# Optimization experiments

Hardware: AMD Instinct MI355X
Metric: run time of the kernel (lower is better)

The kernel has to match this reference:

```python
import jax, jax.numpy as jnp
import numpy as np

B, S, D, P = 8, 2048, 512, 64  # batch, seq, num_embed_hidden, num_attention_project


def setup_inputs() -> dict:
    key = jax.random.key(0)
    ks = jax.random.split(key, 9)
    sd = 1.0 / np.sqrt(D)
    sp = 1.0 / np.sqrt(P)
    return {
        "query": jax.random.normal(ks[0], (B, S, D), dtype=jnp.float32),
        "attention_mask": jnp.ones((B, S), dtype=jnp.float32),
        "Wq": jax.random.uniform(ks[1], (D, P), jnp.float32, -sd, sd),
        "bq": jax.random.uniform(ks[2], (P,), jnp.float32, -sd, sd),
        "Wk": jax.random.uniform(ks[3], (D, P), jnp.float32, -sd, sd),
        "bk": jax.random.uniform(ks[4], (P,), jnp.float32, -sd, sd),
        "Wv": jax.random.uniform(ks[5], (D, P), jnp.float32, -sd, sd),
        "bv": jax.random.uniform(ks[6], (P,), jnp.float32, -sd, sd),
        "Wo": jax.random.uniform(ks[7], (P, D), jnp.float32, -sp, sp),
        "bo": jax.random.uniform(ks[8], (D,), jnp.float32, -sp, sp),
    }


def reference(query, attention_mask, Wq, bq, Wk, bk, Wv, bv, Wo, bo):
    q = jnp.einsum("bsd,dp->bsp", query, Wq) + bq  # [B,S,P]
    k = jnp.einsum("bsd,dp->bsp", query, Wk) + bk
    v = jnp.einsum("bsd,dp->bsp", query, Wv) + bv
    scores = jnp.einsum("bsp,btp->bst", q, k) / jnp.sqrt(jnp.float32(P))  # [B,S,S]
    # Faithful to original: mask broadcast over last axis via unsqueeze(-1) -> masks rows
    scores = scores + (1.0 - attention_mask[:, :, None]) * -10000.0
    weights = jax.nn.softmax(scores, axis=-1)
    weighted = jnp.einsum("bst,btp->bsp", weights, v)
    return jnp.einsum("bsp,pd->bsd", weighted, Wo) + bo
```

## Files before the change

kernel.cpp:

```cpp
#include <hip/hip_runtime.h>
#include <hip/hip_bf16.h>
#include <math.h>

constexpr int B = 8;
constexpr int S = 2048;
constexpr int D = 512;
constexpr int P = 64;
constexpr float SCALE = 0.125f;

typedef short bf16x8 __attribute__((ext_vector_type(8)));
typedef short s16x4 __attribute__((ext_vector_type(4)));
typedef float f32x4 __attribute__((ext_vector_type(4)));

__device__ __forceinline__ unsigned short f2bf(float x) {
  __hip_bfloat16 h = __float2bfloat16(x);
  return __builtin_bit_cast(unsigned short, h);
}
__device__ __forceinline__ float bf2f(unsigned short u) {
  unsigned int v = (unsigned int)u << 16;
  return __builtin_bit_cast(float, v);
}


__global__ __launch_bounds__(256) void prep_w(
    const float* __restrict__ Wq, const float* __restrict__ Wk,
    const float* __restrict__ Wv, const float* __restrict__ Wo,
    unsigned short* __restrict__ Bfrag, unsigned short* __restrict__ Wofrag) {
  const int i = blockIdx.x * 256 + threadIdx.x;
  if (i < 192 * 512) {
    const int d = i / 192;
    const int n = i - d * 192;
    const float* W = (n < 64) ? Wq : (n < 128) ? Wk : Wv;
    const float val = W[d * 64 + (n & 63)];
    const int nt = n >> 4, l15 = n & 15;
    const int k16 = d >> 5, l4 = (d >> 3) & 3, j = d & 7;
    Bfrag[(((nt * 16 + k16) * 4 + l4) * 16 + l15) * 8 + j] = f2bf(val);
  }
  if (i < 64 * 512) {
    const int k = i >> 9;
    const int n = i & 511;
    const float val = Wo[k * 512 + n];
    const int ct = n >> 4, l15 = n & 15;
    const int h = k >> 5, l4 = (k >> 3) & 3, j = k & 7;
    Wofrag[(((ct * 2 + h) * 4 + l4) * 16 + l15) * 8 + j] = f2bf(val);
  }
}

__global__ __launch_bounds__(256)
__attribute__((amdgpu_waves_per_eu(4, 4))) void qkv_mfma(
    const float* __restrict__ query, const unsigned short* __restrict__ Bfrag,
    const float* __restrict__ bq, const float* __restrict__ bk,
    const float* __restrict__ bv, unsigned short* __restrict__ qfrag,
    unsigned short* __restrict__ kfrag, unsigned short* __restrict__ vfrag) {
  __shared__ __align__(16) unsigned short Aq[16 * 512];

  const int tid = threadIdx.x;
  const int w = tid >> 6;
  const int l = tid & 63;
  const int l15 = l & 15;
  const int l4 = l >> 4;
  const int s0 = blockIdx.x * 16;
  const int kb0 = blockIdx.x & 15;

  const float* qsrc = query + (size_t)s0 * D;
#pragma unroll
  for (int step = 0; step < 4; ++step) {
    const int row = step * 4 + w;
    const float* pf = qsrc + row * D + l * 8;
    const float4 x = *(const float4*)pf;
    const float4 y = *(const float4*)(pf + 4);
    bf16x8 u;
    u[0] = (short)f2bf(x.x); u[1] = (short)f2bf(x.y);
    u[2] = (short)f2bf(x.z); u[3] = (short)f2bf(x.w);
    u[4] = (short)f2bf(y.x); u[5] = (short)f2bf(y.y);
    u[6] = (short)f2bf(y.z); u[7] = (short)f2bf(y.w);
    *(bf16x8*)&Aq[row * 512 + ((l ^ (row & 7)) << 3)] = u;
  }
  __syncthreads();

  f32x4 acc[3];
#pragma unroll
  for (int m = 0; m < 3; ++m) acc[m] = (f32x4){0.f, 0.f, 0.f, 0.f};

#pragma unroll
  for (int kk = 0; kk < 16; ++kk) {
    const int k16 = (kk + kb0) & 15;
    const int aslot = (k16 * 4 + l4) ^ (l15 & 7);
    const bf16x8 af = *(const bf16x8*)&Aq[l15 * 512 + (aslot << 3)];
    const bf16x8 bfq =
        *(const bf16x8*)(Bfrag + ((size_t)(w * 16 + k16) * 64 + l) * 8);
    const bf16x8 bfk =
        *(const bf16x8*)(Bfrag + ((size_t)((4 + w) * 16 + k16) * 64 + l) * 8);
    const bf16x8 bfv =
        *(const bf16x8*)(Bfrag + ((size_t)((8 + w) * 16 + k16) * 64 + l) * 8);
    acc[0] = __builtin_amdgcn_mfma_f32_16x16x32_bf16(bfq, af, acc[0], 0, 0, 0);
    acc[1] = __builtin_amdgcn_mfma_f32_16x16x32_bf16(bfk, af, acc[1], 0, 0, 0);
    acc[2] = __builtin_amdgcn_mfma_f32_16x16x32_bf16(af, bfv, acc[2], 0, 0, 0);
  }

  const int bidx = s0 >> 11;
  const size_t bbase = (size_t)bidx * (S * P);
  const int S0 = s0 & 2047;

  const int p0 = w * 16 + l4 * 4;
  const float4 bq4 = *(const float4*)(bq + p0);
  const float4 bk4 = *(const float4*)(bk + p0);
  const size_t qkoff =
      bbase +
      ((((size_t)(S0 >> 4) * 2 + (p0 >> 5)) * 4 + ((p0 >> 3) & 3)) * 16 +
       l15) * 8 +
      (p0 & 7);
  s16x4 pq, pkk;
  pq[0] = (short)f2bf((acc[0][0] + bq4.x) * SCALE);
  pq[1] = (short)f2bf((acc[0][1] + bq4.y) * SCALE);
  pq[2] = (short)f2bf((acc[0][2] + bq4.z) * SCALE);
  pq[3] = (short)f2bf((acc[0][3] + bq4.w) * SCALE);
  pkk[0] = (short)f2bf(acc[1][0] + bk4.x);
  pkk[1] = (short)f2bf(acc[1][1] + bk4.y);
  pkk[2] = (short)f2bf(acc[1][2] + bk4.z);
  pkk[3] = (short)f2bf(acc[1][3] + bk4.w);
  *(s16x4*)(qfrag + qkoff) = pq;
  *(s16x4*)(kfrag + qkoff) = pkk;

  const float bbv = bv[w * 16 + l15];
  const int chv = ((S0 >> 3) + (l4 >> 1)) & 3;
  const size_t voff =
      bbase + ((((size_t)(S0 >> 5) * 4 + w) * 4 + chv) * 16 + l15) * 8 +
      (l4 & 1) * 4;
  s16x4 pv;
  pv[0] = (short)f2bf(acc[2][0] + bbv);
  pv[1] = (short)f2bf(acc[2][1] + bbv);
  pv[2] = (short)f2bf(acc[2][2] + bbv);
  pv[3] = (short)f2bf(acc[2][3] + bbv);
  *(s16x4*)(vfrag + voff) = pv;
}

__global__ __launch_bounds__(1024)
__attribute__((amdgpu_waves_per_eu(4, 4))) void attn_fused(
    const unsigned short* __restrict__ qfrag,
    const unsigned short* __restrict__ kfrag,
    const unsigned short* __restrict__ vfrag,
    const unsigned short* __restrict__ Wofrag, const float* __restrict__ bo,
    float* __restrict__ out) {
  __shared__ __align__(16) unsigned char smem[131072];
  __shared__ float l_s[16][32];

  const int tid = threadIdx.x;
  const int w = tid >> 6;
  const int lane = tid & 63;
  const int l15 = lane & 15;
  const int l4 = lane >> 4;
  const int qg = w & 1;
  const int th = w >> 1;

  const int blk = blockIdx.x;
  const int b = blk & 7;
  const int qt = blk >> 3;
  const int s0 = qt * 64;
  const int wst = qt & 3;

  const size_t bbase = (size_t)b * (S * P);
  const unsigned short* qf = qfrag + bbase;
  const unsigned short* kf = kfrag + bbase;
  const unsigned short* vf = vfrag + bbase;

  unsigned char* e_w = smem + w * 8192;
  const int xm = (l15 & 7) << 4;

  bf16x8 aq[2][2];
#pragma unroll
  for (int st = 0; st < 2; ++st)
#pragma unroll
    for (int h = 0; h < 2; ++h)
      aq[st][h] =
          *(const bf16x8*)(qf +
                           ((size_t)(((s0 >> 4) + qg * 2 + st) * 2 + h) * 64 +
                            lane) *
                               8);

  f32x4 acc[2][4];
#pragma unroll
  for (int st = 0; st < 2; ++st)
#pragma unroll
    for (int pc = 0; pc < 4; ++pc) acc[st][pc] = (f32x4){0.f, 0.f, 0.f, 0.f};
  float lpart[2] = {0.f, 0.f};

  for (int win = 0; win < 4; ++win) {
    const int wi = (win + wst) & 3;
    const int t0 = th * 256 + wi * 64;
    unsigned char* epb = e_w + (win & 1) * 4096;

#pragma unroll 1
    for (int hf = 0; hf < 2; ++hf) {
      bf16x8 bkh[2][2];
#pragma unroll
      for (int j = 0; j < 2; ++j)
#pragma unroll
        for (int h = 0; h < 2; ++h)
          bkh[j][h] =
              *(const bf16x8*)(kf + ((size_t)(((t0 >> 4) + hf * 2 + j) * 2 +
                                              h) * 64 + lane) * 8);

#pragma unroll
      for (int st = 0; st < 2; ++st) {
        f32x4 sc[2];
#pragma unroll
        for (int j = 0; j < 2; ++j) {
          f32x4 c = (f32x4){0.f, 0.f, 0.f, 0.f};
          c = __builtin_amdgcn_mfma_f32_16x16x32_bf16(bkh[j][0], aq[st][0], c,
                                                      0, 0, 0);
          sc[j] = __builtin_amdgcn_mfma_f32_16x16x32_bf16(bkh[j][1], aq[st][1],
                                                          c, 0, 0, 0);
        }
#pragma unroll
        for (int j = 0; j < 2; ++j) {
          s16x4 pk;
#pragma unroll
          for (int r = 0; r < 4; ++r) pk[r] = (short)f2bf(__expf(sc[j][r]));
#pragma unroll
          for (int r = 0; r < 4; ++r)
            lpart[st] += bf2f((unsigned short)pk[r]);
          *(s16x4*)(epb + st * 2048 + l15 * 128 +
                    (((hf * 2 + j) * 32 + l4 * 8) ^ xm)) = pk;
        }
      }

      bf16x8 bvh[4];
#pragma unroll
      for (int pc = 0; pc < 4; ++pc)
        bvh[pc] =
            *(const bf16x8*)(vf + ((size_t)(((t0 >> 5) + hf) * 4 + pc) * 64 +
                                   lane) * 8);

#pragma unroll
      for (int st = 0; st < 2; ++st) {
        const bf16x8 ae = *(const bf16x8*)(epb + st * 2048 + l15 * 128 +
                                           ((hf * 64 + l4 * 16) ^ xm));
#pragma unroll
        for (int pc = 0; pc < 4; ++pc)
          acc[st][pc] = __builtin_amdgcn_mfma_f32_16x16x32_bf16(
              ae, bvh[pc], acc[st][pc], 0, 0, 0);
      }
    }
  }

#pragma unroll
  for (int st = 0; st < 2; ++st) {
    float v = lpart[st];
    v += __shfl_xor(v, 16, 64);
    v += __shfl_xor(v, 32, 64);
    if (l4 == 0) l_s[w][st * 16 + l15] = v;
  }

  __syncthreads();

  float* pacc = (float*)smem;
#pragma unroll
  for (int st = 0; st < 2; ++st)
#pragma unroll
    for (int pc = 0; pc < 4; ++pc)
#pragma unroll
      for (int r = 0; r < 4; ++r) {
        const int row = st * 16 + l4 * 4 + r;
        pacc[((size_t)w * 32 + row) * 64 + ((pc ^ l4) * 16) + l15] =
            acc[st][pc][r];
      }
  __syncthreads();

  const int R = w * 4 + l4;
  const int qgR = R >> 5;
  const int r32 = R & 31;
  const int csw = (r32 >> 2) & 3;
  const int coff = (((l15 >> 2) ^ csw) * 16) + (l15 & 3) * 4;
  float4 s4 = {0.f, 0.f, 0.f, 0.f};
#pragma unroll
  for (int t8 = 0; t8 < 8; ++t8) {
    const float4 p4 =
        *(const float4*)&pacc[((size_t)(t8 * 2 + qgR) * 32 + r32) * 64 + coff];
    s4.x += p4.x; s4.y += p4.y; s4.z += p4.z; s4.w += p4.w;
  }
  float ls = 0.f;
#pragma unroll
  for (int t8 = 0; t8 < 8; ++t8) ls += l_s[t8 * 2 + qgR][r32];
  const float inv = 1.f / ls;
  s16x4 wn;
  wn[0] = (short)f2bf(s4.x * inv);
  wn[1] = (short)f2bf(s4.y * inv);
  wn[2] = (short)f2bf(s4.z * inv);
  wn[3] = (short)f2bf(s4.w * inv);
  __syncthreads();

  unsigned short* wnorm = (unsigned short*)smem;
  *(s16x4*)&wnorm[R * 64 + l15 * 4] = wn;
  __syncthreads();

  const int sub = w & 3;
  const int chq = w >> 2;
  const bf16x8 a0 = *(const bf16x8*)&wnorm[(sub * 16 + l15) * 64 + l4 * 8];
  const bf16x8 a1 =
      *(const bf16x8*)&wnorm[(sub * 16 + l15) * 64 + 32 + l4 * 8];
  const size_t orow0 = (size_t)b * S + s0 + sub * 16;
#pragma unroll
  for (int ct = 0; ct < 8; ++ct) {
    const int ctg = chq * 8 + ((ct + (blk & 7)) & 7);
    const bf16x8 b0 =
        *(const bf16x8*)(Wofrag + ((size_t)(ctg * 2 + 0) * 64 + lane) * 8);
    const bf16x8 b1 =
        *(const bf16x8*)(Wofrag + ((size_t)(ctg * 2 + 1) * 64 + lane) * 8);
    f32x4 c = (f32x4){0.f, 0.f, 0.f, 0.f};
    c = __builtin_amdgcn_mfma_f32_16x16x32_bf16(a0, b0, c, 0, 0, 0);
    c = __builtin_amdgcn_mfma_f32_16x16x32_bf16(a1, b1, c, 0, 0, 0);
    const int col = ctg * 16 + l15;
    const float bb = bo[col];
#pragma unroll
    for (int r = 0; r < 4; ++r)
      out[(orow0 + l4 * 4 + r) * D + col] = c[r] + bb;
  }
}

extern "C" void kernel_launch(void* const* d_in, const int* in_sizes, int n_in,
                              void* d_out, int out_size, void* d_ws,
                              size_t ws_size, hipStream_t stream) {
  const float* query = (const float*)d_in[0];
  const float* Wq = (const float*)d_in[2];
  const float* bq = (const float*)d_in[3];
  const float* Wk = (const float*)d_in[4];
  const float* bk = (const float*)d_in[5];
  const float* Wv = (const float*)d_in[6];
  const float* bv = (const float*)d_in[7];
  const float* Wo = (const float*)d_in[8];
  const float* bo = (const float*)d_in[9];
  float* out = (float*)d_out;

  const size_t proj = (size_t)B * S * P;
  unsigned short* qfr = (unsigned short*)d_ws;
  unsigned short* kfr = qfr + proj;
  unsigned short* vfr = kfr + proj;
  unsigned short* Bfrag = vfr + proj;
  unsigned short* Wofrag = Bfrag + 192 * 512;

  prep_w<<<384, 256, 0, stream>>>(Wq, Wk, Wv, Wo, Bfrag, Wofrag);
  qkv_mfma<<<1024, 256, 0, stream>>>(query, Bfrag, bq, bk, bv, qfr, kfr, vfr);
  attn_fused<<<256, 1024, 0, stream>>>(qfr, kfr, vfr, Wofrag, bo, out);
}
```

Baseline: 124.1 us.

## Halve query tile per block to double grid and cut LDS use

The attention kernel now processes 32 query rows per block instead of 64. Each of the 16 waves covers a distinct 128-key slice, and 512 blocks are launched instead of 256. The cross-wave reduction of partial outputs now runs in two phases over column halves, so LDS drops from 128KB to about 68KB and the waves-per-EU hint is relaxed. The aim is to let two blocks share a CU and to fill all CUs on a 256-CU part. In exchange, each block loads K/V twice as often per query row, adds a barrier-separated reduction phase, and loses the double-buffered exp staging.

```diff
diff --git a/kernel.cpp b/kernel.cpp
--- a/kernel.cpp
+++ b/kernel.cpp
@@ -136,13 +136,13 @@
 }
 
 __global__ __launch_bounds__(1024)
-__attribute__((amdgpu_waves_per_eu(4, 4))) void attn_fused(
+__attribute__((amdgpu_waves_per_eu(8))) void attn_fused(
     const unsigned short* __restrict__ qfrag,
     const unsigned short* __restrict__ kfrag,
     const unsigned short* __restrict__ vfrag,
     const unsigned short* __restrict__ Wofrag, const float* __restrict__ bo,
     float* __restrict__ out) {
-  __shared__ __align__(16) unsigned char smem[131072];
+  __shared__ __align__(16) unsigned char smem[69632];
   __shared__ float l_s[16][32];
 
   const int tid = threadIdx.x;
@@ -150,21 +150,19 @@
   const int lane = tid & 63;
   const int l15 = lane & 15;
   const int l4 = lane >> 4;
-  const int qg = w & 1;
-  const int th = w >> 1;
 
   const int blk = blockIdx.x;
   const int b = blk & 7;
   const int qt = blk >> 3;
-  const int s0 = qt * 64;
-  const int wst = qt & 3;
+  const int s0 = qt * 32;
+  const int wst = qt & 1;
 
   const size_t bbase = (size_t)b * (S * P);
   const unsigned short* qf = qfrag + bbase;
   const unsigned short* kf = kfrag + bbase;
   const unsigned short* vf = vfrag + bbase;
 
-  unsigned char* e_w = smem + w * 8192;
+  unsigned char* e_w = smem + w * 4096;
   const int xm = (l15 & 7) << 4;
 
   bf16x8 aq[2][2];
@@ -174,9 +172,7 @@
     for (int h = 0; h < 2; ++h)
       aq[st][h] =
           *(const bf16x8*)(qf +
-                           ((size_t)(((s0 >> 4) + qg * 2 + st) * 2 + h) * 64 +
-                            lane) *
-                               8);
+                           ((size_t)((qt * 2 + st) * 2 + h) * 64 + lane) * 8);
 
   f32x4 acc[2][4];
 #pragma unroll
@@ -185,10 +181,10 @@
     for (int pc = 0; pc < 4; ++pc) acc[st][pc] = (f32x4){0.f, 0.f, 0.f, 0.f};
   float lpart[2] = {0.f, 0.f};
 
-  for (int win = 0; win < 4; ++win) {
-    const int wi = (win + wst) & 3;
-    const int t0 = th * 256 + wi * 64;
-    unsigned char* epb = e_w + (win & 1) * 4096;
+  for (int win = 0; win < 2; ++win) {
+    const int wi = (win + wst) & 1;
+    const int t0 = w * 128 + wi * 64;
+    unsigned char* epb = e_w;
 
 #pragma unroll 1
     for (int hf = 0; hf < 2; ++hf) {
@@ -255,54 +251,48 @@
   __syncthreads();
 
   float* pacc = (float*)smem;
-#pragma unroll
-  for (int st = 0; st < 2; ++st)
-#pragma unroll
-    for (int pc = 0; pc < 4; ++pc)
-#pragma unroll
-      for (int r = 0; r < 4; ++r) {
-        const int row = st * 16 + l4 * 4 + r;
-        pacc[((size_t)w * 32 + row) * 64 + ((pc ^ l4) * 16) + l15] =
-            acc[st][pc][r];
+  unsigned short* wnorm = (unsigned short*)(smem + 65536);
+
+  const int crow = (w & 7) * 4 + l4;
+  const int prel = (w >> 3) * 16 + l15;
+  const int rc = (((w >> 3) ^ (w & 1)) << 4) + l15;
+  float ls = 0.f;
+#pragma unroll
+  for (int s2 = 0; s2 < 16; ++s2) ls += l_s[s2][crow];
+  const float inv = 1.f / ls;
+
+#pragma unroll 1
+  for (int ph = 0; ph < 2; ++ph) {
+#pragma unroll
+    for (int st = 0; st < 2; ++st)
+#pragma unroll
+      for (int pcx = 0; pcx < 2; ++pcx) {
+        const int pc = ph * 2 + pcx;
+        const int cs = ((pcx ^ (l4 & 1)) << 4) + l15;
+#pragma unroll
+        for (int r = 0; r < 4; ++r) {
+          const int row = st * 16 + l4 * 4 + r;
+          pacc[(w * 32 + row) * 32 + cs] = acc[st][pc][r];
+        }
       }
-  __syncthreads();
-
-  const int R = w * 4 + l4;
-  const int qgR = R >> 5;
-  const int r32 = R & 31;
-  const int csw = (r32 >> 2) & 3;
-  const int coff = (((l15 >> 2) ^ csw) * 16) + (l15 & 3) * 4;
-  float4 s4 = {0.f, 0.f, 0.f, 0.f};
-#pragma unroll
-  for (int t8 = 0; t8 < 8; ++t8) {
-    const float4 p4 =
-        *(const float4*)&pacc[((size_t)(t8 * 2 + qgR) * 32 + r32) * 64 + coff];
-    s4.x += p4.x; s4.y += p4.y; s4.z += p4.z; s4.w += p4.w;
-  }
-  float ls = 0.f;
-#pragma unroll
-  for (int t8 = 0; t8 < 8; ++t8) ls += l_s[t8 * 2 + qgR][r32];
-  const float inv = 1.f / ls;
-  s16x4 wn;
-  wn[0] = (short)f2bf(s4.x * inv);
-  wn[1] = (short)f2bf(s4.y * inv);
-  wn[2] = (short)f2bf(s4.z * inv);
-  wn[3] = (short)f2bf(s4.w * inv);
-  __syncthreads();
-
-  unsigned short* wnorm = (unsigned short*)smem;
-  *(s16x4*)&wnorm[R * 64 + l15 * 4] = wn;
-  __syncthreads();
-
-  const int sub = w & 3;
-  const int chq = w >> 2;
+    __syncthreads();
+
+    float s = 0.f;
+#pragma unroll
+    for (int s2 = 0; s2 < 16; ++s2) s += pacc[(s2 * 32 + crow) * 32 + rc];
+    wnorm[crow * 64 + ph * 32 + prel] = f2bf(s * inv);
+    __syncthreads();
+  }
+
+  const int sub = w & 1;
+  const int chq = w >> 1;
   const bf16x8 a0 = *(const bf16x8*)&wnorm[(sub * 16 + l15) * 64 + l4 * 8];
   const bf16x8 a1 =
       *(const bf16x8*)&wnorm[(sub * 16 + l15) * 64 + 32 + l4 * 8];
   const size_t orow0 = (size_t)b * S + s0 + sub * 16;
 #pragma unroll
-  for (int ct = 0; ct < 8; ++ct) {
-    const int ctg = chq * 8 + ((ct + (blk & 7)) & 7);
+  for (int ct = 0; ct < 4; ++ct) {
+    const int ctg = chq * 4 + ((ct + (blk & 3)) & 3);
     const bf16x8 b0 =
         *(const bf16x8*)(Wofrag + ((size_t)(ctg * 2 + 0) * 64 + lane) * 8);
     const bf16x8 b1 =
@@ -341,5 +331,5 @@
 
   prep_w<<<384, 256, 0, stream>>>(Wq, Wk, Wv, Wo, Bfrag, Wofrag);
   qkv_mfma<<<1024, 256, 0, stream>>>(query, Bfrag, bq, bk, bv, qfr, kfr, vfr);
-  attn_fused<<<256, 1024, 0, stream>>>(qfr, kfr, vfr, Wofrag, bo, out);
-}
+  attn_fused<<<512, 1024, 0, stream>>>(qfr, kfr, vfr, Wofrag, bo, out);
+}
```

New measurement: 212.9 us. 71.5% more time.
